# Optimization experiments

Measured on AMD Instinct MI355X. Metric: run time of the kernel, lower is better.

The kernel has to match this reference:

```python
import jax, jax.numpy as jnp
from jax import lax
import numpy as np

MAX_ITER = 12      # sifting iterations per IMF
TOL = 0.05         # sd tolerance / flatness tolerance
NUM_IMFS = 6       # max IMFs extracted
EPS = 1e-8


def _peak_mask(s):
    # strict local maxima, matching scipy.signal.find_peaks on plateau-free
    # (continuous random) signals: s[i-1] < s[i] > s[i+1]
    interior = (s[:, 1:-1] > s[:, :-2]) & (s[:, 1:-1] > s[:, 2:])
    return jnp.pad(interior, ((0, 0), (1, 1)))  # [B, L] bool


def _interp_env(s, mask):
    # piecewise-linear interpolation through masked peaks, flat extrapolation
    # at the ends (np.interp with left=first peak val, right=last peak val)
    B, L = s.shape
    idx = jnp.arange(L)
    last = lax.cummax(jnp.where(mask, idx, -1), axis=1)               # prev peak idx (-1 if none)
    nxt = lax.cummin(jnp.where(mask, idx, L), axis=1, reverse=True)   # next peak idx (L if none)
    vl = jnp.take_along_axis(s, jnp.clip(last, 0, L - 1), axis=1)
    vr = jnp.take_along_axis(s, jnp.clip(nxt, 0, L - 1), axis=1)
    denom = nxt - last
    frac = jnp.where(denom > 0,
                     (idx - last).astype(s.dtype) / jnp.maximum(denom, 1).astype(s.dtype),
                     jnp.zeros((), s.dtype))
    env = vl + frac * (vr - vl)
    env = jnp.where(last < 0, vr, env)   # left of first peak
    env = jnp.where(nxt >= L, vl, env)   # right of last peak
    return env


def _envelope(s, upper):
    mask = _peak_mask(s) if upper else _peak_mask(-s)
    env = _interp_env(s, mask)
    # fallback when fewer than 2 peaks: running max / running min of s
    fb = lax.cummax(s, axis=1) if upper else lax.cummin(s, axis=1)
    few = mask.sum(axis=1, keepdims=True) < 2
    return jnp.where(few, fb, env)


def _extract_imf(signal):
    # iterative sifting with early-stop masked into a fixed-length scan
    def body(carry, _):
        h, done = carry
        mean = 0.5 * (_envelope(h, True) + _envelope(h, False))
        # sd = sum((h - h_new)^2) / (sum(h^2)+eps) and h - h_new == mean
        sd = jnp.sum(mean ** 2) / (jnp.sum(h ** 2) + EPS)
        conv = sd < TOL
        h_next = jnp.where(done | conv, h, h - mean)
        return (h_next, done | conv), None
    (h, _), _ = lax.scan(body, (signal, jnp.array(False)), None, length=MAX_ITER)
    return h, signal - h


def _emd(x):
    def step(carry, _):
        res, done = carry
        imf, new_res = _extract_imf(res)
        imf = jnp.where(done, jnp.zeros_like(imf), imf)
        new_res = jnp.where(done, res, new_res)
        # _is_residual_flat: var(diff) < tol * var(residual) (torch.var unbiased)
        d = jnp.diff(new_res, axis=-1)
        flat = jnp.var(d, ddof=1) < TOL * jnp.var(new_res, ddof=1)
        return (new_res, done | flat), imf
    (res, _), imfs = lax.scan(step, (x, jnp.array(False)), None, length=NUM_IMFS)
    # stack IMFs and residual: [NUM_IMFS+1, B, L]; IMFs after early stop are zeros
    return jnp.concatenate([imfs, res[None]], axis=0)


def setup_inputs() -> dict:
    key = jax.random.key(0)
    x = jax.random.normal(key, (64, 16384), dtype=jnp.float32)
    return {"x": x}


def reference(x):
    return _emd(x)
```

## Files before the change

kernel.cpp:

```cpp
#include <hip/hip_runtime.h>

#define NL 16384
#define NB 64
#define NT 1024
#define NC (NL / NT)
#define NW (NT / 64)
#define N_ITER 12
#define N_IMFS 6

#pragma clang fp contract(off)

#define HSZ (NL + (NL >> 5))
__device__ __forceinline__ int physi(int i) { return i + (i >> 5); }

#define FMAXV 3.402823466e38f

__global__ __launch_bounds__(NT, 4) void emd_main(
    const float* __restrict__ x, float* __restrict__ out, char* __restrict__ ws) {
  unsigned* scnt = (unsigned*)ws;
  double*   sdsl = (double*)(ws + 512);
  unsigned* fcnt = (unsigned*)(ws + 2048);
  double*   flsl = (double*)(ws + 2304);

  __shared__ float hbuf[2 * HSZ];
  __shared__ int wLU[NW], wLL[NW], wNU[NW], wNL[NW];
  __shared__ float wMx[NW], wMn[NW];
  __shared__ unsigned wCT[NW];
  __shared__ int eLU[NW], eLL[NW], eNU[NW], eNL[NW];
  __shared__ float eMx[NW], eMn[NW];
  __shared__ unsigned sTot;
  __shared__ double tA[NW], tB[NW], tC[NW], tD[NW];
  __shared__ int sFlag;

  const int t = threadIdx.x;
  const int lane = t & 63;
  const int wv = t >> 6;
  const int row = blockIdx.x;
  const int base = t * NC;
  const float* xr = x + (size_t)row * NL;
  float* res = out + (size_t)N_IMFS * NB * NL + (size_t)row * NL;

  int off = 0;

  #pragma unroll
  for (int q = 0; q < NC / 4; q++) {
    int i0 = base + q * 4;
    float4 v = *(const float4*)&xr[i0];
    *(float4*)&hbuf[physi(i0)] = v;
    *(float4*)&res[i0] = v;
  }
  __syncthreads();

  bool done = false;

  for (int k = 0; k < N_IMFS; k++) {
    float* outk = out + (size_t)k * NB * NL + (size_t)row * NL;
    if (done) {
      #pragma unroll
      for (int q = 0; q < NC / 4; q++)
        *(float4*)&outk[base + q * 4] = make_float4(0.f, 0.f, 0.f, 0.f);
      continue;
    }

    int fin = 0;
    for (int it = 0; it < N_ITER; it++) {
      if (it >= 1) {
        if (t == 0) {
          int s = k * N_ITER + (it - 1);
          while (__hip_atomic_load(&scnt[s], __ATOMIC_ACQUIRE, __HIP_MEMORY_SCOPE_AGENT) < NB)
            __builtin_amdgcn_s_sleep(1);
          double m2 = __hip_atomic_load(&sdsl[s * 2 + 0], __ATOMIC_RELAXED, __HIP_MEMORY_SCOPE_AGENT);
          double h2 = __hip_atomic_load(&sdsl[s * 2 + 1], __ATOMIC_RELAXED, __HIP_MEMORY_SCOPE_AGENT);
          sFlag = (m2 / (h2 + 1e-8) < 0.05) ? 1 : 0;
        }
        __syncthreads();
        if (sFlag) { off ^= HSZ; fin = 1; break; }
      }
      float* hcur = hbuf + off;
      float* hnx  = hbuf + (off ^ HSZ);

      unsigned mU = 0, mL = 0;
      int lmU = -1, lmL = -1, cU = 0, cL = 0;
      float rmx = -FMAXV, rmn = FMAXV;
      {
        float hm = (base > 0) ? hcur[physi(base - 1)] : 0.0f;
        float4 cur = *(const float4*)&hcur[physi(base)];
        #define PKSTEP(J, HC, HP) { int i = base + (J);                     \
          bool in = (i > 0) && (i + 1 < NL);                                \
          if (in && hm < (HC) && (HC) > (HP)) { mU |= 1u << (J); lmU = i; cU++; } \
          if (in && hm > (HC) && (HC) < (HP)) { mL |= 1u << (J); lmL = i; cL++; } \
          rmx = fmaxf(rmx, (HC)); rmn = fminf(rmn, (HC)); hm = (HC); }
        #pragma unroll
        for (int q = 0; q < 4; q++) {
          float4 nxt = cur;
          float n0;
          if (q < 3) { nxt = *(const float4*)&hcur[physi(base + q * 4 + 4)]; n0 = nxt.x; }
          else       { n0 = (base + 16 < NL) ? hcur[physi(base + 16)] : 0.0f; }
          PKSTEP(q * 4 + 0, cur.x, cur.y)
          PKSTEP(q * 4 + 1, cur.y, cur.z)
          PKSTEP(q * 4 + 2, cur.z, cur.w)
          PKSTEP(q * 4 + 3, cur.w, n0)
          cur = nxt;
        }
        #undef PKSTEP
      }
      int fpU = mU ? (base + __ffs(mU) - 1) : NL;
      int fpL = mL ? (base + __ffs(mL) - 1) : NL;
      unsigned long long bUm = __ballot(mU != 0);
      unsigned long long bLm = __ballot(mL != 0);
      {
        int s;
        s = bUm ? (63 - __clzll((long long)bUm)) : 0;
        if (lane == s) wLU[wv] = bUm ? lmU : -1;
        s = bLm ? (63 - __clzll((long long)bLm)) : 0;
        if (lane == s) wLL[wv] = bLm ? lmL : -1;
        s = bUm ? (__ffsll(bUm) - 1) : 0;
        if (lane == s) wNU[wv] = bUm ? fpU : NL;
        s = bLm ? (__ffsll(bLm) - 1) : 0;
        if (lane == s) wNL[wv] = bLm ? fpL : NL;
      }
      unsigned ict = ((unsigned)cU << 16) | (unsigned)cL;
      #pragma unroll
      for (int o = 1; o < 64; o <<= 1) {
        unsigned cc = __shfl_down(ict, o, 64);
        if (lane + o < 64) ict += cc;
      }
      if (lane == 0) wCT[wv] = ict;
      __syncthreads();
      if (t == 0) {
        int aLU = -1, aLL = -1; unsigned tt = 0;
        for (int w = 0; w < NW; w++) {
          eLU[w] = aLU; aLU = max(aLU, wLU[w]);
          eLL[w] = aLL; aLL = max(aLL, wLL[w]);
          tt += wCT[w];
        }
        int aNU = NL, aNL = NL;
        for (int w = NW - 1; w >= 0; w--) {
          eNU[w] = aNU; aNU = min(aNU, wNU[w]);
          eNL[w] = aNL; aNL = min(aNL, wNL[w]);
        }
        sTot = tt;
      }
      __syncthreads();
      const unsigned tot = sTot;
      const int totU = (int)(tot >> 16), totL = (int)(tot & 0xffffu);

      unsigned long long belowU = bUm & ((1ull << lane) - 1ull);
      unsigned long long belowL = bLm & ((1ull << lane) - 1ull);
      unsigned long long aboveU = (lane == 63) ? 0ull : (bUm & (~0ull << (lane + 1)));
      unsigned long long aboveL = (lane == 63) ? 0ull : (bLm & (~0ull << (lane + 1)));
      int slU = belowU ? (63 - __clzll((long long)belowU)) : 0;
      int slL = belowL ? (63 - __clzll((long long)belowL)) : 0;
      int snU = aboveU ? (__ffsll(aboveU) - 1) : 0;
      int snL = aboveL ? (__ffsll(aboveL) - 1) : 0;
      int gU  = __shfl(lmU, slU, 64);
      int gL  = __shfl(lmL, slL, 64);
      int gNU = __shfl(fpU, snU, 64);
      int gNL = __shfl(fpL, snL, 64);
      const int clU = belowU ? gU  : eLU[wv];
      const int clL = belowL ? gL  : eLL[wv];
      const int cnU = aboveU ? gNU : eNU[wv];
      const int cnL = aboveL ? gNL : eNL[wv];

      float crx = -FMAXV, crn = FMAXV;
      if (totU < 2 || totL < 2) {
        float iMx = rmx, iMn = rmn;
        #pragma unroll
        for (int o = 1; o < 64; o <<= 1) {
          float fa = __shfl_up(iMx, o, 64);
          float fb = __shfl_up(iMn, o, 64);
          if (lane >= o) { iMx = fmaxf(iMx, fa); iMn = fminf(iMn, fb); }
        }
        if (lane == 63) { wMx[wv] = iMx; wMn[wv] = iMn; }
        __syncthreads();
        if (t == 0) {
          float aMx = -FMAXV, aMn = FMAXV;
          for (int w = 0; w < NW; w++) {
            eMx[w] = aMx; aMx = fmaxf(aMx, wMx[w]);
            eMn[w] = aMn; aMn = fminf(aMn, wMn[w]);
          }
        }
        __syncthreads();
        float pMx = __shfl_up(iMx, 1, 64); if (lane == 0) pMx = -FMAXV;
        float pMn = __shfl_up(iMn, 1, 64); if (lane == 0) pMn = FMAXV;
        crx = fmaxf(eMx[wv], pMx);
        crn = fminf(eMn[wv], pMn);
      }

      double pm2 = 0.0, ph2 = 0.0;
      {
        float rx = crx, rn = crn;
        int curLU = clU, curLL = clL;
        float vl = hcur[physi(clU < 0 ? 0 : clU)];
        float wl = hcur[physi(clL < 0 ? 0 : clL)];
        int gB = -0x7fffffff, gD = -0x7fffffff;
        float vr = 0.0f, wr = 0.0f;
        #define ENVSTEP(J, HC, OD) { int i = base + (J); float hc = (HC);   \
          rx = fmaxf(rx, hc); rn = fminf(rn, hc);                           \
          if ((mU >> (J)) & 1u) { curLU = i; vl = hc; }                     \
          if ((mL >> (J)) & 1u) { curLL = i; wl = hc; }                     \
          int lU = curLU, lL = curLL;                                       \
          unsigned highm = 0xFFFFFFFFu << (J); unsigned a;                  \
          a = mU & highm; int nUv = a ? (base + __ffs(a) - 1) : cnU;        \
          a = mL & highm; int nLv = a ? (base + __ffs(a) - 1) : cnL;        \
          if (nUv != gB) { gB = nUv; vr = hcur[physi(nUv >= NL ? NL - 1 : nUv)]; } \
          if (nLv != gD) { gD = nLv; wr = hcur[physi(nLv >= NL ? NL - 1 : nLv)]; } \
          int den = nUv - lU;                                               \
          float fracU = (float)(i - lU) / (float)(den > 0 ? den : 1);       \
          float envU = (den > 0) ? __builtin_fmaf(fracU, vr - vl, vl) : vl; \
          if (lU < 0) envU = vr;                                            \
          if (nUv >= NL) envU = vl;                                         \
          if (totU < 2) envU = rx;                                          \
          int den2 = nLv - lL;                                              \
          float fracL = (float)(i - lL) / (float)(den2 > 0 ? den2 : 1);     \
          float envL = (den2 > 0) ? __builtin_fmaf(fracL, wr - wl, wl) : wl;\
          if (lL < 0) envL = wr;                                            \
          if (nLv >= NL) envL = wl;                                         \
          if (totL < 2) envL = rn;                                          \
          float mn = 0.5f * (envU + envL);                                  \
          (OD) = hc - mn;                                                   \
          pm2 += (double)mn * (double)mn; ph2 += (double)hc * (double)hc; }
        #pragma unroll
        for (int q = 0; q < 4; q++) {
          int i0 = base + q * 4;
          float4 hv4 = *(const float4*)&hcur[physi(i0)];
          float4 o4;
          ENVSTEP(q * 4 + 0, hv4.x, o4.x)
          ENVSTEP(q * 4 + 1, hv4.y, o4.y)
          ENVSTEP(q * 4 + 2, hv4.z, o4.z)
          ENVSTEP(q * 4 + 3, hv4.w, o4.w)
          *(float4*)&hnx[physi(i0)] = o4;
        }
        #undef ENVSTEP
      }
      #pragma unroll
      for (int o = 1; o < 64; o <<= 1) {
        double a = __shfl_down(pm2, o, 64);
        double b = __shfl_down(ph2, o, 64);
        if (lane + o < 64) { pm2 += a; ph2 += b; }
      }
      if (lane == 0) { tA[wv] = pm2; tB[wv] = ph2; }
      __syncthreads();
      if (t == 0) {
        double sA = 0.0, sB = 0.0;
        for (int w = 0; w < NW; w++) { sA += tA[w]; sB += tB[w]; }
        int s = k * N_ITER + it;
        atomicAdd(&sdsl[s * 2 + 0], sA);
        atomicAdd(&sdsl[s * 2 + 1], sB);
        __hip_atomic_fetch_add(&scnt[s], 1u, __ATOMIC_ACQ_REL, __HIP_MEMORY_SCOPE_AGENT);
      }
      off ^= HSZ;
    }
    if (!fin) {
      if (t == 0) {
        int s = k * N_ITER + (N_ITER - 1);
        while (__hip_atomic_load(&scnt[s], __ATOMIC_ACQUIRE, __HIP_MEMORY_SCOPE_AGENT) < NB)
          __builtin_amdgcn_s_sleep(1);
        double m2 = __hip_atomic_load(&sdsl[s * 2 + 0], __ATOMIC_RELAXED, __HIP_MEMORY_SCOPE_AGENT);
        double h2 = __hip_atomic_load(&sdsl[s * 2 + 1], __ATOMIC_RELAXED, __HIP_MEMORY_SCOPE_AGENT);
        sFlag = (m2 / (h2 + 1e-8) < 0.05) ? 1 : 0;
      }
      __syncthreads();
      if (sFlag) off ^= HSZ;
    }

    float* hcur = hbuf + off;

    if (k > 0) {
      if (t == 0) {
        while (__hip_atomic_load(&fcnt[k - 1], __ATOMIC_ACQUIRE, __HIP_MEMORY_SCOPE_AGENT) < NB)
          __builtin_amdgcn_s_sleep(1);
        double S1 = __hip_atomic_load(&flsl[(k - 1) * 4 + 0], __ATOMIC_RELAXED, __HIP_MEMORY_SCOPE_AGENT);
        double S2 = __hip_atomic_load(&flsl[(k - 1) * 4 + 1], __ATOMIC_RELAXED, __HIP_MEMORY_SCOPE_AGENT);
        double S3 = __hip_atomic_load(&flsl[(k - 1) * 4 + 2], __ATOMIC_RELAXED, __HIP_MEMORY_SCOPE_AGENT);
        double S4 = __hip_atomic_load(&flsl[(k - 1) * 4 + 3], __ATOMIC_RELAXED, __HIP_MEMORY_SCOPE_AGENT);
        double nr = (double)NB * (double)NL;
        double nd = (double)NB * (double)(NL - 1);
        double varr = (S2 - S1 * S1 / nr) / (nr - 1.0);
        double vard = (S4 - S3 * S3 / nd) / (nd - 1.0);
        sFlag = (vard < 0.05 * varr) ? 1 : 0;
      }
      __syncthreads();
      if (sFlag) done = true;
    }
    if (done) {
      #pragma unroll
      for (int q = 0; q < NC / 4; q++)
        *(float4*)&outk[base + q * 4] = make_float4(0.f, 0.f, 0.f, 0.f);
      continue;
    }

    double s1 = 0.0, s2 = 0.0, s3 = 0.0, s4 = 0.0;
    {
      float rb = 0.0f;
      if (base + NC < NL) rb = res[base + NC] - hcur[physi(base + NC)];
      float4 rv4 = *(const float4*)&res[base];
      float4 hv4 = *(const float4*)&hcur[physi(base)];
      float e0 = rv4.x - hv4.x, e1 = rv4.y - hv4.y,
            e2 = rv4.z - hv4.z, e3 = rv4.w - hv4.w;
      #define FLSTEP(J, CUR, NXT) { int i = base + (J);                     \
        s1 += (double)(CUR); s2 += (double)(CUR) * (double)(CUR);           \
        if (i + 1 < NL) { float dd = (NXT) - (CUR);                         \
          s3 += (double)dd; s4 += (double)dd * (double)dd; } }
      #pragma unroll
      for (int q = 0; q < 4; q++) {
        float c0 = e0, c1 = e1, c2 = e2, c3 = e3;
        float n0;
        if (q < 3) {
          int i0 = base + q * 4 + 4;
          rv4 = *(const float4*)&res[i0];
          hv4 = *(const float4*)&hcur[physi(i0)];
          e0 = rv4.x - hv4.x; e1 = rv4.y - hv4.y;
          e2 = rv4.z - hv4.z; e3 = rv4.w - hv4.w;
          n0 = e0;
        } else n0 = rb;
        FLSTEP(q * 4 + 0, c0, c1)
        FLSTEP(q * 4 + 1, c1, c2)
        FLSTEP(q * 4 + 2, c2, c3)
        FLSTEP(q * 4 + 3, c3, n0)
      }
      #undef FLSTEP
    }
    #pragma unroll
    for (int o = 1; o < 64; o <<= 1) {
      double a = __shfl_down(s1, o, 64);
      double b = __shfl_down(s2, o, 64);
      double c = __shfl_down(s3, o, 64);
      double d = __shfl_down(s4, o, 64);
      if (lane + o < 64) { s1 += a; s2 += b; s3 += c; s4 += d; }
    }
    if (lane == 0) { tA[wv] = s1; tB[wv] = s2; tC[wv] = s3; tD[wv] = s4; }
    __syncthreads();
    if (t == 0) {
      double S1 = 0.0, S2 = 0.0, S3 = 0.0, S4 = 0.0;
      for (int w = 0; w < NW; w++) { S1 += tA[w]; S2 += tB[w]; S3 += tC[w]; S4 += tD[w]; }
      atomicAdd(&flsl[k * 4 + 0], S1);
      atomicAdd(&flsl[k * 4 + 1], S2);
      atomicAdd(&flsl[k * 4 + 2], S3);
      atomicAdd(&flsl[k * 4 + 3], S4);
      __hip_atomic_fetch_add(&fcnt[k], 1u, __ATOMIC_ACQ_REL, __HIP_MEMORY_SCOPE_AGENT);
    }
    #pragma unroll
    for (int q = 0; q < NC / 4; q++) {
      int i0 = base + q * 4;
      int p0 = physi(i0);
      float4 rv = *(const float4*)&res[i0];
      float4 hv = *(const float4*)&hcur[p0];
      float4 rq = make_float4(rv.x - hv.x, rv.y - hv.y, rv.z - hv.z, rv.w - hv.w);
      *(float4*)&outk[i0] = hv;
      *(float4*)&res[i0] = rq;
      *(float4*)&hcur[p0] = rq;
    }
    __syncthreads();
  }
}

extern "C" void kernel_launch(void* const* d_in, const int* in_sizes, int n_in,
                              void* d_out, int out_size, void* d_ws, size_t ws_size,
                              hipStream_t stream) {
  const float* x = (const float*)d_in[0];
  float* out = (float*)d_out;
  size_t zb = ws_size < 4096 ? ws_size : 4096;
  hipMemsetAsync(d_ws, 0, zb, stream);
  hipLaunchKernelGGL(emd_main, dim3(NB), dim3(NT), 0, stream,
                     x, out, (char*)d_ws);
}
```

Measured before the change: 330.6 us.

## Defer global convergence check by one iteration using a ring buffer of sifted states

The per-iteration grid-wide wait on the sd convergence reduction is moved later and checked with a lag of two iterations, so each block can keep sifting speculatively instead of stalling on the slowest block. Recent h states are saved to a 3-slot per-row ring in global workspace so the correct state can be restored when convergence is found late. The check is also merged into an existing thread-0 serial section, removing one barrier. Global counters and accumulators are padded to separate cache lines to cut false sharing. In exchange it adds extra global writes every iteration, a restore copy on early stop, and a dependence on workspace size, falling back to lag one if the workspace is too small.

```diff
diff --git a/kernel.cpp b/kernel.cpp
--- a/kernel.cpp
+++ b/kernel.cpp
@@ -16,11 +16,13 @@
 #define FMAXV 3.402823466e38f
 
 __global__ __launch_bounds__(NT, 4) void emd_main(
-    const float* __restrict__ x, float* __restrict__ out, char* __restrict__ ws) {
+    const float* __restrict__ x, float* __restrict__ out, char* __restrict__ ws,
+    int useRing) {
   unsigned* scnt = (unsigned*)ws;
-  double*   sdsl = (double*)(ws + 512);
-  unsigned* fcnt = (unsigned*)(ws + 2048);
-  double*   flsl = (double*)(ws + 2304);
+  double*   sdsl = (double*)(ws + 8192);
+  unsigned* fcnt = (unsigned*)(ws + 16384);
+  double*   flsl = (double*)(ws + 20480);
+  float*    ring = (float*)(ws + 32768);
 
   __shared__ float hbuf[2 * HSZ];
   __shared__ int wLU[NW], wLL[NW], wNU[NW], wNL[NW];
@@ -39,6 +41,8 @@
   const int base = t * NC;
   const float* xr = x + (size_t)row * NL;
   float* res = out + (size_t)N_IMFS * NB * NL + (size_t)row * NL;
+  float* myring = ring + (size_t)row * 3 * NL;
+  const int LAG = useRing ? 2 : 1;
 
   int off = 0;
 
@@ -64,18 +68,6 @@
 
     int fin = 0;
     for (int it = 0; it < N_ITER; it++) {
-      if (it >= 1) {
-        if (t == 0) {
-          int s = k * N_ITER + (it - 1);
-          while (__hip_atomic_load(&scnt[s], __ATOMIC_ACQUIRE, __HIP_MEMORY_SCOPE_AGENT) < NB)
-            __builtin_amdgcn_s_sleep(1);
-          double m2 = __hip_atomic_load(&sdsl[s * 2 + 0], __ATOMIC_RELAXED, __HIP_MEMORY_SCOPE_AGENT);
-          double h2 = __hip_atomic_load(&sdsl[s * 2 + 1], __ATOMIC_RELAXED, __HIP_MEMORY_SCOPE_AGENT);
-          sFlag = (m2 / (h2 + 1e-8) < 0.05) ? 1 : 0;
-        }
-        __syncthreads();
-        if (sFlag) { off ^= HSZ; fin = 1; break; }
-      }
       float* hcur = hbuf + off;
       float* hnx  = hbuf + (off ^ HSZ);
 
@@ -140,8 +132,34 @@
           eNL[w] = aNL; aNL = min(aNL, wNL[w]);
         }
         sTot = tt;
+        int flag = 0;
+        if (it >= LAG) {
+          int s = k * N_ITER + (it - LAG);
+          while (__hip_atomic_load(&scnt[s * 16], __ATOMIC_ACQUIRE, __HIP_MEMORY_SCOPE_AGENT) < NB)
+            __builtin_amdgcn_s_sleep(1);
+          double m2 = __hip_atomic_load(&sdsl[s * 8 + 0], __ATOMIC_RELAXED, __HIP_MEMORY_SCOPE_AGENT);
+          double h2 = __hip_atomic_load(&sdsl[s * 8 + 1], __ATOMIC_RELAXED, __HIP_MEMORY_SCOPE_AGENT);
+          flag = (m2 / (h2 + 1e-8) < 0.05) ? 1 : 0;
+        }
+        sFlag = flag;
       }
       __syncthreads();
+      if (sFlag) {
+        int j = it - LAG;
+        if (useRing) {
+          const float* src = (j == 0) ? res : (myring + (size_t)(j % 3) * NL);
+          #pragma unroll
+          for (int q = 0; q < 4; q++) {
+            int i0 = base + q * 4;
+            float4 v = *(const float4*)&src[i0];
+            *(float4*)&hcur[physi(i0)] = v;
+          }
+          __syncthreads();
+        } else {
+          off ^= HSZ;
+        }
+        fin = 1; break;
+      }
       const unsigned tot = sTot;
       const int totU = (int)(tot >> 16), totL = (int)(tot & 0xffffu);
 
@@ -187,6 +205,7 @@
         crn = fminf(eMn[wv], pMn);
       }
 
+      float* rdst = myring + (size_t)((it + 1) % 3) * NL;
       double pm2 = 0.0, ph2 = 0.0;
       {
         float rx = crx, rn = crn;
@@ -230,6 +249,7 @@
           ENVSTEP(q * 4 + 2, hv4.z, o4.z)
           ENVSTEP(q * 4 + 3, hv4.w, o4.w)
           *(float4*)&hnx[physi(i0)] = o4;
+          if (useRing) *(float4*)&rdst[i0] = o4;
         }
         #undef ENVSTEP
       }
@@ -245,35 +265,52 @@
         double sA = 0.0, sB = 0.0;
         for (int w = 0; w < NW; w++) { sA += tA[w]; sB += tB[w]; }
         int s = k * N_ITER + it;
-        atomicAdd(&sdsl[s * 2 + 0], sA);
-        atomicAdd(&sdsl[s * 2 + 1], sB);
-        __hip_atomic_fetch_add(&scnt[s], 1u, __ATOMIC_ACQ_REL, __HIP_MEMORY_SCOPE_AGENT);
+        atomicAdd(&sdsl[s * 8 + 0], sA);
+        atomicAdd(&sdsl[s * 8 + 1], sB);
+        __hip_atomic_fetch_add(&scnt[s * 16], 1u, __ATOMIC_ACQ_REL, __HIP_MEMORY_SCOPE_AGENT);
       }
       off ^= HSZ;
     }
     if (!fin) {
-      if (t == 0) {
-        int s = k * N_ITER + (N_ITER - 1);
-        while (__hip_atomic_load(&scnt[s], __ATOMIC_ACQUIRE, __HIP_MEMORY_SCOPE_AGENT) < NB)
-          __builtin_amdgcn_s_sleep(1);
-        double m2 = __hip_atomic_load(&sdsl[s * 2 + 0], __ATOMIC_RELAXED, __HIP_MEMORY_SCOPE_AGENT);
-        double h2 = __hip_atomic_load(&sdsl[s * 2 + 1], __ATOMIC_RELAXED, __HIP_MEMORY_SCOPE_AGENT);
-        sFlag = (m2 / (h2 + 1e-8) < 0.05) ? 1 : 0;
-      }
-      __syncthreads();
-      if (sFlag) off ^= HSZ;
+      for (int j = N_ITER - LAG; j < N_ITER; j++) {
+        if (t == 0) {
+          int s = k * N_ITER + j;
+          while (__hip_atomic_load(&scnt[s * 16], __ATOMIC_ACQUIRE, __HIP_MEMORY_SCOPE_AGENT) < NB)
+            __builtin_amdgcn_s_sleep(1);
+          double m2 = __hip_atomic_load(&sdsl[s * 8 + 0], __ATOMIC_RELAXED, __HIP_MEMORY_SCOPE_AGENT);
+          double h2 = __hip_atomic_load(&sdsl[s * 8 + 1], __ATOMIC_RELAXED, __HIP_MEMORY_SCOPE_AGENT);
+          sFlag = (m2 / (h2 + 1e-8) < 0.05) ? 1 : 0;
+        }
+        __syncthreads();
+        if (sFlag) {
+          if (useRing) {
+            const float* src = myring + (size_t)(j % 3) * NL;
+            float* hc = hbuf + off;
+            #pragma unroll
+            for (int q = 0; q < 4; q++) {
+              int i0 = base + q * 4;
+              float4 v = *(const float4*)&src[i0];
+              *(float4*)&hc[physi(i0)] = v;
+            }
+            __syncthreads();
+          } else {
+            off ^= HSZ;
+          }
+          break;
+        }
+      }
     }
 
     float* hcur = hbuf + off;
 
     if (k > 0) {
       if (t == 0) {
-        while (__hip_atomic_load(&fcnt[k - 1], __ATOMIC_ACQUIRE, __HIP_MEMORY_SCOPE_AGENT) < NB)
+        while (__hip_atomic_load(&fcnt[(k - 1) * 16], __ATOMIC_ACQUIRE, __HIP_MEMORY_SCOPE_AGENT) < NB)
           __builtin_amdgcn_s_sleep(1);
-        double S1 = __hip_atomic_load(&flsl[(k - 1) * 4 + 0], __ATOMIC_RELAXED, __HIP_MEMORY_SCOPE_AGENT);
-        double S2 = __hip_atomic_load(&flsl[(k - 1) * 4 + 1], __ATOMIC_RELAXED, __HIP_MEMORY_SCOPE_AGENT);
-        double S3 = __hip_atomic_load(&flsl[(k - 1) * 4 + 2], __ATOMIC_RELAXED, __HIP_MEMORY_SCOPE_AGENT);
-        double S4 = __hip_atomic_load(&flsl[(k - 1) * 4 + 3], __ATOMIC_RELAXED, __HIP_MEMORY_SCOPE_AGENT);
+        double S1 = __hip_atomic_load(&flsl[(k - 1) * 8 + 0], __ATOMIC_RELAXED, __HIP_MEMORY_SCOPE_AGENT);
+        double S2 = __hip_atomic_load(&flsl[(k - 1) * 8 + 1], __ATOMIC_RELAXED, __HIP_MEMORY_SCOPE_AGENT);
+        double S3 = __hip_atomic_load(&flsl[(k - 1) * 8 + 2], __ATOMIC_RELAXED, __HIP_MEMORY_SCOPE_AGENT);
+        double S4 = __hip_atomic_load(&flsl[(k - 1) * 8 + 3], __ATOMIC_RELAXED, __HIP_MEMORY_SCOPE_AGENT);
         double nr = (double)NB * (double)NL;
         double nd = (double)NB * (double)(NL - 1);
         double varr = (S2 - S1 * S1 / nr) / (nr - 1.0);
@@ -334,11 +371,11 @@
     if (t == 0) {
       double S1 = 0.0, S2 = 0.0, S3 = 0.0, S4 = 0.0;
       for (int w = 0; w < NW; w++) { S1 += tA[w]; S2 += tB[w]; S3 += tC[w]; S4 += tD[w]; }
-      atomicAdd(&flsl[k * 4 + 0], S1);
-      atomicAdd(&flsl[k * 4 + 1], S2);
-      atomicAdd(&flsl[k * 4 + 2], S3);
-      atomicAdd(&flsl[k * 4 + 3], S4);
-      __hip_atomic_fetch_add(&fcnt[k], 1u, __ATOMIC_ACQ_REL, __HIP_MEMORY_SCOPE_AGENT);
+      atomicAdd(&flsl[k * 8 + 0], S1);
+      atomicAdd(&flsl[k * 8 + 1], S2);
+      atomicAdd(&flsl[k * 8 + 2], S3);
+      atomicAdd(&flsl[k * 8 + 3], S4);
+      __hip_atomic_fetch_add(&fcnt[k * 16], 1u, __ATOMIC_ACQ_REL, __HIP_MEMORY_SCOPE_AGENT);
     }
     #pragma unroll
     for (int q = 0; q < NC / 4; q++) {
@@ -360,8 +397,10 @@
                               hipStream_t stream) {
   const float* x = (const float*)d_in[0];
   float* out = (float*)d_out;
-  size_t zb = ws_size < 4096 ? ws_size : 4096;
+  size_t needed = 32768 + (size_t)NB * 3 * NL * sizeof(float);
+  int useRing = (ws_size >= needed) ? 1 : 0;
+  size_t zb = ws_size < 32768 ? ws_size : 32768;
   hipMemsetAsync(d_ws, 0, zb, stream);
   hipLaunchKernelGGL(emd_main, dim3(NB), dim3(NT), 0, stream,
-                     x, out, (char*)d_ws);
+                     x, out, (char*)d_ws, useRing);
 }
```

Result: slower. 382.0 us (+15.5%).
